# Performance work log

Measured on AMD Instinct MI355X. Metric: run time of the kernel, lower is better.

## Reference

```python
import jax, jax.numpy as jnp
import numpy as np
from jax import lax

B, S, H = 2, 2048, 768
FF = 1536
E = 8
TOP_K = 2


def setup_inputs() -> dict:
    key = jax.random.key(0)
    k1, k2, k3, k4 = jax.random.split(key, 4)
    hidden_states = jax.random.normal(k1, (B, S, H), dtype=jnp.float32)
    # torch init: weight.normal_() for experts; nn.Linear default init for gate (approx normal here is fine for a numerics baseline)
    gate_w = jax.random.normal(k2, (E, H), dtype=jnp.float32) * 0.02
    w_fc = jax.random.normal(k3, (E, FF, H), dtype=jnp.float32) * 0.02
    w_proj = jax.random.normal(k4, (E, H, FF), dtype=jnp.float32) * 0.02
    return {"hidden_states": hidden_states, "gate_w": gate_w, "w_fc": w_fc, "w_proj": w_proj}


def reference(hidden_states, gate_w, w_fc, w_proj):
    b, s, h = hidden_states.shape
    x = hidden_states.reshape(-1, h)                      # [T, H]
    # --- top-k gating (logits in float32, as in the torch code) ---
    logits = (x @ gate_w.T).astype(jnp.float32)           # [T, E]
    top_logits, top_idx = lax.top_k(logits, TOP_K)        # [T, K]
    gates = jax.nn.softmax(top_logits, axis=1).astype(x.dtype)  # [T, K]
    # combined per-token/per-expert gate: g[t,e] = sum_k gates[t,k]*[idx[t,k]==e]
    onehot = jax.nn.one_hot(top_idx, E, dtype=x.dtype)    # [T, K, E]
    g = jnp.einsum('tk,tke->te', gates, onehot)           # [T, E]
    # --- experts: gather + per-expert GEMM + gated scatter-add combine ---
    # Equivalent math: tokens with zero gate for expert e contribute nothing,
    # so compute each expert on all tokens and weight by g[:, e].
    out = jnp.zeros_like(x)
    for e in range(E):  # fixed small loop over experts (structurally distinct weights)
        hmid = jax.nn.gelu(x @ w_fc[e].T, approximate=False)   # [T, FF] (torch gelu = erf form)
        out = out + g[:, e:e + 1] * (hmid @ w_proj[e].T)       # [T, H]
    out = out.reshape(b, s, h)
    return out, logits
```

## Files before the change

### kernel.cpp

```cpp
#include <hip/hip_runtime.h>
#include <hip/hip_bf16.h>
#include <math.h>
#include <stdint.h>

#define TOKENS 4096
#define HDIM   768
#define FFDIM  1536
#define NEXP   8
#define GEMM_GRID 1024
#define SLOTS (GEMM_GRID / 8)

typedef __attribute__((ext_vector_type(8))) short bf16x8;
typedef __attribute__((ext_vector_type(4))) float f32x4;

__device__ __forceinline__ unsigned short f2bf(float f) {
    union { float f; uint32_t u; } c; c.f = f;
    uint32_t u = c.u;
    uint32_t r = (u + 0x7FFFu + ((u >> 16) & 1u)) >> 16;
    return (unsigned short)r;
}

__device__ __forceinline__ void gload_lds16(const void* g, void* l) {
    __builtin_amdgcn_global_load_lds(
        (const __attribute__((address_space(1))) void*)g,
        (__attribute__((address_space(3))) void*)l, 16, 0, 0);
}

__global__ void cast_bf16_2(const float* __restrict__ s1, unsigned short* __restrict__ d1,
                            const float* __restrict__ s2, unsigned short* __restrict__ d2,
                            int n4) {
    int stride = gridDim.x * blockDim.x;
    for (int i = blockIdx.x * blockDim.x + threadIdx.x; i < 2 * n4; i += stride) {
        const float4* s = (i < n4) ? (const float4*)s1 : (const float4*)s2;
        ushort4* d = (i < n4) ? (ushort4*)d1 : (ushort4*)d2;
        int j = (i < n4) ? i : i - n4;
        float4 v = s[j];
        ushort4 o;
        o.x = f2bf(v.x); o.y = f2bf(v.y); o.z = f2bf(v.z); o.w = f2bf(v.w);
        d[j] = o;
    }
}

__global__ __launch_bounds__(256) void gating(
    const float* __restrict__ x, const float* __restrict__ gw,
    float* __restrict__ logits,
    int* __restrict__ tok_e, float* __restrict__ tok_g,
    unsigned short* __restrict__ x_bf, float* __restrict__ outp)
{
    float4 zz = make_float4(0.f, 0.f, 0.f, 0.f);
#pragma unroll
    for (int j = 0; j < 3; j++)
        ((float4*)outp)[blockIdx.x * 768 + j * 256 + threadIdx.x] = zz;

    int t = blockIdx.x * 4 + (threadIdx.x >> 6);
    int lane = threadIdx.x & 63;
    const float4* xt = (const float4*)(x + (size_t)t * HDIM);
    const float4* gw4 = (const float4*)gw;
    ushort4* xbt = (ushort4*)(x_bf + (size_t)t * HDIM);
    float acc[NEXP];
#pragma unroll
    for (int e = 0; e < NEXP; e++) acc[e] = 0.f;
#pragma unroll
    for (int it = 0; it < 3; it++) {
        int i = lane + it * 64;
        float4 xv = xt[i];
        ushort4 o;
        o.x = f2bf(xv.x); o.y = f2bf(xv.y); o.z = f2bf(xv.z); o.w = f2bf(xv.w);
        xbt[i] = o;
#pragma unroll
        for (int e = 0; e < NEXP; e++) {
            float4 wv = gw4[e * 192 + i];
            acc[e] += xv.x * wv.x + xv.y * wv.y + xv.z * wv.z + xv.w * wv.w;
        }
    }
#pragma unroll
    for (int e = 0; e < NEXP; e++) {
#pragma unroll
        for (int off = 32; off > 0; off >>= 1)
            acc[e] += __shfl_xor(acc[e], off);
    }
    if (lane == 0) {
        float4 l0 = make_float4(acc[0], acc[1], acc[2], acc[3]);
        float4 l1 = make_float4(acc[4], acc[5], acc[6], acc[7]);
        float4* lp = (float4*)(logits + (size_t)t * NEXP);
        lp[0] = l0; lp[1] = l1;
        int i0 = 0; float v0 = acc[0];
#pragma unroll
        for (int e = 1; e < NEXP; e++) if (acc[e] > v0) { v0 = acc[e]; i0 = e; }
        int i1 = -1; float v1 = -3.4e38f;
#pragma unroll
        for (int e = 0; e < NEXP; e++) if (e != i0 && acc[e] > v1) { v1 = acc[e]; i1 = e; }
        float g0 = 1.f / (1.f + expf(v1 - v0));
        tok_e[t * 2] = i0; tok_e[t * 2 + 1] = i1;
        tok_g[t * 2] = g0; tok_g[t * 2 + 1] = 1.f - g0;
    }
}

__global__ __launch_bounds__(1024) void build_lists(
    const int* __restrict__ tok_e, const float* __restrict__ tok_g,
    int* __restrict__ counts,
    int* __restrict__ entries, float* __restrict__ gates)
{
    __shared__ unsigned long long wlo[16], whi[16];
    int tid = threadIdx.x;
    int lane = tid & 63, wid = tid >> 6;

    int eL[8]; float gL[8];
    int4 ea = ((const int4*)tok_e)[tid * 2];
    int4 eb = ((const int4*)tok_e)[tid * 2 + 1];
    float4 ga = ((const float4*)tok_g)[tid * 2];
    float4 gb = ((const float4*)tok_g)[tid * 2 + 1];
    eL[0] = ea.x; eL[1] = ea.y; eL[2] = ea.z; eL[3] = ea.w;
    eL[4] = eb.x; eL[5] = eb.y; eL[6] = eb.z; eL[7] = eb.w;
    gL[0] = ga.x; gL[1] = ga.y; gL[2] = ga.z; gL[3] = ga.w;
    gL[4] = gb.x; gL[5] = gb.y; gL[6] = gb.z; gL[7] = gb.w;

    unsigned long long clo = 0, chi = 0;
#pragma unroll
    for (int j = 0; j < 8; j++) {
        int e = eL[j];
        unsigned long long one = 1ull << ((e & 3) * 16);
        if (e < 4) clo += one; else chi += one;
    }
    unsigned long long ilo = clo, ihi = chi;
#pragma unroll
    for (int s = 1; s < 64; s <<= 1) {
        unsigned long long t1 = __shfl_up(ilo, s);
        unsigned long long t2 = __shfl_up(ihi, s);
        if (lane >= s) { ilo += t1; ihi += t2; }
    }
    if (lane == 63) { wlo[wid] = ilo; whi[wid] = ihi; }
    __syncthreads();
    if (tid == 0) {
        unsigned long long rl = 0, rh = 0;
#pragma unroll
        for (int i = 0; i < 16; i++) {
            unsigned long long a = wlo[i], b = whi[i];
            wlo[i] = rl; whi[i] = rh;
            rl += a; rh += b;
        }
#pragma unroll
        for (int e = 0; e < 4; e++) {
            counts[e]     = (int)((rl >> (e * 16)) & 0xFFFF);
            counts[e + 4] = (int)((rh >> (e * 16)) & 0xFFFF);
        }
    }
    __syncthreads();
    unsigned long long rlo = wlo[wid] + (ilo - clo);
    unsigned long long rhi = whi[wid] + (ihi - chi);
#pragma unroll
    for (int j = 0; j < 8; j++) {
        int e = eL[j];
        int sh = (e & 3) * 16;
        unsigned long long one = 1ull << sh;
        int slot;
        if (e < 4) { slot = (int)((rlo >> sh) & 0xFFFF); rlo += one; }
        else       { slot = (int)((rhi >> sh) & 0xFFFF); rhi += one; }
        entries[e * TOKENS + slot] = tid * 8 + j;
        gates[e * TOKENS + slot]   = gL[j];
    }
}

template<int KD, int ND, int TN, int NCTP, bool IS_FC, bool DBUF>
__global__ __launch_bounds__(512) void moe_gemm(
    const unsigned short* __restrict__ Asrc,
    const unsigned short* __restrict__ Bsrc,
    const int* __restrict__ counts,
    const int* __restrict__ entries,
    const float* __restrict__ gates,
    unsigned short* __restrict__ hmid,
    float* __restrict__ outp)
{
    constexpr int BM = 256;
    constexpr int AJ = TN / 32;
    constexpr int CB = TN / 64;
    constexpr int NV = 4 + CB;
    int bkt  = blockIdx.x & 7;
    int slot = blockIdx.x >> 3;

    int cs[NEXP];
#pragma unroll
    for (int e = 0; e < NEXP; e++) cs[e] = counts[e];
    int n_e = cs[bkt];
    int rts = (n_e + BM - 1) >> 8;
    int nfill = rts * NCTP;
    if (slot >= nfill) return;
    int ebase = 0;
#pragma unroll
    for (int e = 0; e < NEXP; e++) if (e < bkt) ebase += cs[e];
    const int* lst = entries + bkt * TOKENS;

    int tid = threadIdx.x;
    int w = tid >> 6;
    int l = tid & 63;
    int sg = l & 7;
    int lr8 = l >> 3;
    int lo = l & 15;
    int q  = l >> 4;
    int wr = w >> 1, wc = w & 1;

    __shared__ __align__(16) unsigned short sA[(DBUF ? 2 : 1) * BM * 64];
    __shared__ __align__(16) unsigned short sB[(DBUF ? 2 : 1) * TN * 64];
    unsigned short* sA0 = sA;
    unsigned short* sA1 = sA + BM * 64;
    unsigned short* sB0 = sB;
    unsigned short* sB1 = sB + TN * 64;

    int aOff[4][2], bOff[AJ][2];
#pragma unroll
    for (int i = 0; i < 4; i++) {
        int m = wr * 64 + i * 16 + lo;
#pragma unroll
        for (int s = 0; s < 2; s++)
            aOff[i][s] = m * 64 + ((s * 4 + q) ^ (m & 7)) * 8;
    }
#pragma unroll
    for (int j = 0; j < AJ; j++) {
        int n = wc * (TN / 2) + j * 16 + lo;
#pragma unroll
        for (int s = 0; s < 2; s++)
            bOff[j][s] = n * 64 + ((s * 4 + q) ^ (n & 7)) * 8;
    }

    for (int p = slot; p < nfill; p += SLOTS) {
        int ct   = p / rts;
        int r    = p - ct * rts;
        int row0 = r << 8;
        int n0 = ct * TN;

        const unsigned short* Ag[4];
        int aLds[4];
#pragma unroll
        for (int c = 0; c < 4; c++) {
            int rr = w * 32 + c * 8 + lr8;
            int gr = row0 + rr;
            int id = gr < n_e ? gr : n_e - 1;
            size_t arow = IS_FC ? (size_t)(lst[id] >> 1) : (size_t)(ebase + id);
            Ag[c] = Asrc + arow * KD + (size_t)((sg ^ (rr & 7)) * 8);
            aLds[c] = (w * 32 + c * 8) * 64;
        }
        const unsigned short* Bg[CB];
        int bLds[CB];
#pragma unroll
        for (int c = 0; c < CB; c++) {
            int rr = w * (TN / 8) + c * 8 + lr8;
            Bg[c] = Bsrc + ((size_t)bkt * ND + n0 + rr) * KD + (size_t)((sg ^ (rr & 7)) * 8);
            bLds[c] = (w * (TN / 8) + c * 8) * 64;
        }

        f32x4 acc[4][AJ];
#pragma unroll
        for (int i = 0; i < 4; i++)
#pragma unroll
            for (int j = 0; j < AJ; j++) acc[i][j] = (f32x4){0.f, 0.f, 0.f, 0.f};

        auto stage = [&](unsigned short* SA, unsigned short* SB, int k0) {
#pragma unroll
            for (int c = 0; c < 4; c++) gload_lds16(Ag[c] + k0, SA + aLds[c]);
#pragma unroll
            for (int c = 0; c < CB; c++) gload_lds16(Bg[c] + k0, SB + bLds[c]);
        };
        auto compute = [&](const unsigned short* SA, const unsigned short* SB) {
#pragma unroll
            for (int s = 0; s < 2; s++) {
                bf16x8 a[4], b[AJ];
#pragma unroll
                for (int i = 0; i < 4; i++) a[i] = *(const bf16x8*)(SA + aOff[i][s]);
#pragma unroll
                for (int j = 0; j < AJ; j++) b[j] = *(const bf16x8*)(SB + bOff[j][s]);
#pragma unroll
                for (int i = 0; i < 4; i++)
#pragma unroll
                    for (int j = 0; j < AJ; j++)
                        acc[i][j] = __builtin_amdgcn_mfma_f32_16x16x32_bf16(a[i], b[j], acc[i][j], 0, 0, 0);
            }
        };

        if constexpr (!DBUF) {
            for (int k0 = 0; k0 < KD; k0 += 64) {
                stage(sA0, sB0, k0);
                __syncthreads();
                compute(sA0, sB0);
                __syncthreads();
            }
        } else {
#define WAITN asm volatile("s_waitcnt vmcnt(%0)" :: "n"(NV) : "memory")
#define WAIT0 asm volatile("s_waitcnt vmcnt(0)" ::: "memory")
            stage(sA0, sB0, 0);
            for (int k0 = 0; k0 < KD; k0 += 128) {
                stage(sA1, sB1, k0 + 64);
                WAITN;
                __builtin_amdgcn_s_barrier();
                __builtin_amdgcn_s_setprio(1);
                compute(sA0, sB0);
                __builtin_amdgcn_s_setprio(0);
                __builtin_amdgcn_s_barrier();
                if (k0 + 128 < KD) {
                    stage(sA0, sB0, k0 + 128);
                    WAITN;
                } else {
                    WAIT0;
                }
                __builtin_amdgcn_s_barrier();
                __builtin_amdgcn_s_setprio(1);
                compute(sA1, sB1);
                __builtin_amdgcn_s_setprio(0);
                __builtin_amdgcn_s_barrier();
            }
#undef WAITN
#undef WAIT0
        }

#pragma unroll
        for (int i = 0; i < 4; i++) {
            int rowB = row0 + wr * 64 + i * 16 + q * 4;
#pragma unroll
            for (int rr = 0; rr < 4; rr++) {
                int orow = rowB + rr;
                if (orow < n_e) {
                    if (IS_FC) {
                        size_t hrow = (size_t)(ebase + orow);
#pragma unroll
                        for (int j = 0; j < AJ; j++) {
                            float v = acc[i][j][rr];
                            v = 0.5f * v * (1.f + erff(v * 0.70710678118654752f));
                            hmid[hrow * ND + n0 + wc * (TN / 2) + j * 16 + lo] = f2bf(v);
                        }
                    } else {
                        int token = lst[orow] >> 1;
                        float g = gates[bkt * TOKENS + orow];
#pragma unroll
                        for (int j = 0; j < AJ; j++) {
                            atomicAdd(&outp[(size_t)token * ND + n0 + wc * (TN / 2) + j * 16 + lo],
                                      acc[i][j][rr] * g);
                        }
                    }
                }
            }
        }
    }
}

extern "C" void kernel_launch(void* const* d_in, const int* in_sizes, int n_in,
                              void* d_out, int out_size, void* d_ws, size_t ws_size,
                              hipStream_t stream) {
    const float* x     = (const float*)d_in[0];
    const float* gw    = (const float*)d_in[1];
    const float* wfc   = (const float*)d_in[2];
    const float* wproj = (const float*)d_in[3];
    float* outp   = (float*)d_out;
    float* logits = outp + (size_t)TOKENS * HDIM;

    char* ws = (char*)d_ws;
    int*   counts  = (int*)ws;
    size_t off = 256;
    int*   entries = (int*)(ws + off);
    float* gates   = (float*)(ws + off + NEXP * TOKENS * 4);
    off += 2ull * NEXP * TOKENS * 4;
    int*   tok_e   = (int*)(ws + off);   off += (size_t)TOKENS * 2 * 4;
    float* tok_g   = (float*)(ws + off); off += (size_t)TOKENS * 2 * 4;
    unsigned short* x_bf   = (unsigned short*)(ws + off); off += (size_t)TOKENS * HDIM * 2;
    unsigned short* wfc_bf = (unsigned short*)(ws + off); off += (size_t)NEXP * FFDIM * HDIM * 2;
    unsigned short* wpj_bf = (unsigned short*)(ws + off); off += (size_t)NEXP * HDIM * FFDIM * 2;
    unsigned short* hmid   = (unsigned short*)(ws + off);

    cast_bf16_2<<<2048, 256, 0, stream>>>(wfc, wfc_bf, wproj, wpj_bf,
                                          NEXP * FFDIM * HDIM / 4);
    gating<<<TOKENS / 4, 256, 0, stream>>>(x, gw, logits, tok_e, tok_g, x_bf, outp);
    build_lists<<<1, 1024, 0, stream>>>(tok_e, tok_g, counts, entries, gates);
    moe_gemm<HDIM, FFDIM, 128, FFDIM / 128, true,  false><<<GEMM_GRID, 512, 0, stream>>>(
        x_bf, wfc_bf, counts, entries, gates, hmid, outp);
    moe_gemm<FFDIM, HDIM, 64,  HDIM / 64,   false, true ><<<GEMM_GRID, 512, 0, stream>>>(
        hmid, wpj_bf, counts, entries, gates, hmid, outp);
}
```

Baseline: 223.0 us.

## Fuse weight cast into gating kernel; double-buffer FC GEMM with BK=32

Merges the weight fp32-to-bf16 cast and the gating kernel into one launch, using extra blocks for the cast, which removes a kernel launch and lets the two run concurrently. It also generalizes the MoE GEMM to a template K-tile size and makes the FC GEMM double-buffered with BK=32 tiles. The smaller tile keeps the doubled LDS footprint in check, and the swizzle is adapted for 4-chunk rows. The cost is more barriers per K step for the FC GEMM, and gating blocks now share the GPU with the bandwidth-heavy cast.

Result: no change. 225.3 us (+1.1%).

```diff
diff --git a/kernel.cpp b/kernel.cpp
--- a/kernel.cpp
+++ b/kernel.cpp
@@ -26,27 +26,27 @@
         (__attribute__((address_space(3))) void*)l, 16, 0, 0);
 }
 
-__global__ void cast_bf16_2(const float* __restrict__ s1, unsigned short* __restrict__ d1,
-                            const float* __restrict__ s2, unsigned short* __restrict__ d2,
-                            int n4) {
-    int stride = gridDim.x * blockDim.x;
-    for (int i = blockIdx.x * blockDim.x + threadIdx.x; i < 2 * n4; i += stride) {
-        const float4* s = (i < n4) ? (const float4*)s1 : (const float4*)s2;
-        ushort4* d = (i < n4) ? (ushort4*)d1 : (ushort4*)d2;
-        int j = (i < n4) ? i : i - n4;
-        float4 v = s[j];
-        ushort4 o;
-        o.x = f2bf(v.x); o.y = f2bf(v.y); o.z = f2bf(v.z); o.w = f2bf(v.w);
-        d[j] = o;
-    }
-}
-
-__global__ __launch_bounds__(256) void gating(
+__global__ __launch_bounds__(256) void cast_gate(
     const float* __restrict__ x, const float* __restrict__ gw,
+    const float* __restrict__ wfc, const float* __restrict__ wproj,
+    unsigned short* __restrict__ wfc_bf, unsigned short* __restrict__ wpj_bf,
     float* __restrict__ logits,
     int* __restrict__ tok_e, float* __restrict__ tok_g,
-    unsigned short* __restrict__ x_bf, float* __restrict__ outp)
+    unsigned short* __restrict__ x_bf, float* __restrict__ outp, int n4)
 {
+    if (blockIdx.x >= 1024) {
+        int stride = 2048 * 256;
+        for (int i = (blockIdx.x - 1024) * 256 + threadIdx.x; i < 2 * n4; i += stride) {
+            const float4* s = (i < n4) ? (const float4*)wfc : (const float4*)wproj;
+            ushort4* d = (i < n4) ? (ushort4*)wfc_bf : (ushort4*)wpj_bf;
+            int j = (i < n4) ? i : i - n4;
+            float4 v = s[j];
+            ushort4 o;
+            o.x = f2bf(v.x); o.y = f2bf(v.y); o.z = f2bf(v.z); o.w = f2bf(v.w);
+            d[j] = o;
+        }
+        return;
+    }
     float4 zz = make_float4(0.f, 0.f, 0.f, 0.f);
 #pragma unroll
     for (int j = 0; j < 3; j++)
@@ -161,7 +161,7 @@
     }
 }
 
-template<int KD, int ND, int TN, int NCTP, bool IS_FC, bool DBUF>
+template<int KD, int ND, int BK, int TN, int NCTP, bool IS_FC>
 __global__ __launch_bounds__(512) void moe_gemm(
     const unsigned short* __restrict__ Asrc,
     const unsigned short* __restrict__ Bsrc,
@@ -173,8 +173,16 @@
 {
     constexpr int BM = 256;
     constexpr int AJ = TN / 32;
-    constexpr int CB = TN / 64;
-    constexpr int NV = 4 + CB;
+    constexpr int S  = BK / 8;
+    constexpr int RPC = 64 / S;
+    constexpr int LS  = (S == 8) ? 3 : 2;
+    constexpr int SH  = (S == 8) ? 0 : 1;
+    constexpr int MK  = S - 1;
+    constexpr int ACAL = 32 / RPC;
+    constexpr int BCAL = (TN / 8) / RPC;
+    constexpr int NV   = ACAL + BCAL;
+    constexpr int SS   = BK / 32;
+
     int bkt  = blockIdx.x & 7;
     int slot = blockIdx.x >> 3;
 
@@ -193,33 +201,33 @@
     int tid = threadIdx.x;
     int w = tid >> 6;
     int l = tid & 63;
-    int sg = l & 7;
-    int lr8 = l >> 3;
+    int sg = l & MK;
+    int lr = l >> LS;
     int lo = l & 15;
     int q  = l >> 4;
     int wr = w >> 1, wc = w & 1;
 
-    __shared__ __align__(16) unsigned short sA[(DBUF ? 2 : 1) * BM * 64];
-    __shared__ __align__(16) unsigned short sB[(DBUF ? 2 : 1) * TN * 64];
+    __shared__ __align__(16) unsigned short sA[2 * BM * BK];
+    __shared__ __align__(16) unsigned short sB[2 * TN * BK];
     unsigned short* sA0 = sA;
-    unsigned short* sA1 = sA + BM * 64;
+    unsigned short* sA1 = sA + BM * BK;
     unsigned short* sB0 = sB;
-    unsigned short* sB1 = sB + TN * 64;
-
-    int aOff[4][2], bOff[AJ][2];
+    unsigned short* sB1 = sB + TN * BK;
+
+    int aOff[4][SS], bOff[AJ][SS];
 #pragma unroll
     for (int i = 0; i < 4; i++) {
         int m = wr * 64 + i * 16 + lo;
 #pragma unroll
-        for (int s = 0; s < 2; s++)
-            aOff[i][s] = m * 64 + ((s * 4 + q) ^ (m & 7)) * 8;
+        for (int s = 0; s < SS; s++)
+            aOff[i][s] = m * BK + (((s * 4 + q) ^ ((m >> SH) & MK)) * 8);
     }
 #pragma unroll
     for (int j = 0; j < AJ; j++) {
         int n = wc * (TN / 2) + j * 16 + lo;
 #pragma unroll
-        for (int s = 0; s < 2; s++)
-            bOff[j][s] = n * 64 + ((s * 4 + q) ^ (n & 7)) * 8;
+        for (int s = 0; s < SS; s++)
+            bOff[j][s] = n * BK + (((s * 4 + q) ^ ((n >> SH) & MK)) * 8);
     }
 
     for (int p = slot; p < nfill; p += SLOTS) {
@@ -228,24 +236,24 @@
         int row0 = r << 8;
         int n0 = ct * TN;
 
-        const unsigned short* Ag[4];
-        int aLds[4];
-#pragma unroll
-        for (int c = 0; c < 4; c++) {
-            int rr = w * 32 + c * 8 + lr8;
+        const unsigned short* Ag[ACAL];
+        int aLds[ACAL];
+#pragma unroll
+        for (int c = 0; c < ACAL; c++) {
+            int rr = w * 32 + c * RPC + lr;
             int gr = row0 + rr;
             int id = gr < n_e ? gr : n_e - 1;
             size_t arow = IS_FC ? (size_t)(lst[id] >> 1) : (size_t)(ebase + id);
-            Ag[c] = Asrc + arow * KD + (size_t)((sg ^ (rr & 7)) * 8);
-            aLds[c] = (w * 32 + c * 8) * 64;
-        }
-        const unsigned short* Bg[CB];
-        int bLds[CB];
-#pragma unroll
-        for (int c = 0; c < CB; c++) {
-            int rr = w * (TN / 8) + c * 8 + lr8;
-            Bg[c] = Bsrc + ((size_t)bkt * ND + n0 + rr) * KD + (size_t)((sg ^ (rr & 7)) * 8);
-            bLds[c] = (w * (TN / 8) + c * 8) * 64;
+            Ag[c] = Asrc + arow * KD + (size_t)((sg ^ ((rr >> SH) & MK)) * 8);
+            aLds[c] = (w * 32 + c * RPC) * BK;
+        }
+        const unsigned short* Bg[BCAL];
+        int bLds[BCAL];
+#pragma unroll
+        for (int c = 0; c < BCAL; c++) {
+            int rr = w * (TN / 8) + c * RPC + lr;
+            Bg[c] = Bsrc + ((size_t)bkt * ND + n0 + rr) * KD + (size_t)((sg ^ ((rr >> SH) & MK)) * 8);
+            bLds[c] = (w * (TN / 8) + c * RPC) * BK;
         }
 
         f32x4 acc[4][AJ];
@@ -256,13 +264,13 @@
 
         auto stage = [&](unsigned short* SA, unsigned short* SB, int k0) {
 #pragma unroll
-            for (int c = 0; c < 4; c++) gload_lds16(Ag[c] + k0, SA + aLds[c]);
-#pragma unroll
-            for (int c = 0; c < CB; c++) gload_lds16(Bg[c] + k0, SB + bLds[c]);
+            for (int c = 0; c < ACAL; c++) gload_lds16(Ag[c] + k0, SA + aLds[c]);
+#pragma unroll
+            for (int c = 0; c < BCAL; c++) gload_lds16(Bg[c] + k0, SB + bLds[c]);
         };
         auto compute = [&](const unsigned short* SA, const unsigned short* SB) {
 #pragma unroll
-            for (int s = 0; s < 2; s++) {
+            for (int s = 0; s < SS; s++) {
                 bf16x8 a[4], b[AJ];
 #pragma unroll
                 for (int i = 0; i < 4; i++) a[i] = *(const bf16x8*)(SA + aOff[i][s]);
@@ -276,40 +284,31 @@
             }
         };
 
-        if constexpr (!DBUF) {
-            for (int k0 = 0; k0 < KD; k0 += 64) {
-                stage(sA0, sB0, k0);
-                __syncthreads();
-                compute(sA0, sB0);
-                __syncthreads();
-            }
-        } else {
 #define WAITN asm volatile("s_waitcnt vmcnt(%0)" :: "n"(NV) : "memory")
 #define WAIT0 asm volatile("s_waitcnt vmcnt(0)" ::: "memory")
-            stage(sA0, sB0, 0);
-            for (int k0 = 0; k0 < KD; k0 += 128) {
-                stage(sA1, sB1, k0 + 64);
+        stage(sA0, sB0, 0);
+        for (int k0 = 0; k0 < KD; k0 += 2 * BK) {
+            stage(sA1, sB1, k0 + BK);
+            WAITN;
+            __builtin_amdgcn_s_barrier();
+            __builtin_amdgcn_s_setprio(1);
+            compute(sA0, sB0);
+            __builtin_amdgcn_s_setprio(0);
+            __builtin_amdgcn_s_barrier();
+            if (k0 + 2 * BK < KD) {
+                stage(sA0, sB0, k0 + 2 * BK);
                 WAITN;
-                __builtin_amdgcn_s_barrier();
-                __builtin_amdgcn_s_setprio(1);
-                compute(sA0, sB0);
-                __builtin_amdgcn_s_setprio(0);
-                __builtin_amdgcn_s_barrier();
-                if (k0 + 128 < KD) {
-                    stage(sA0, sB0, k0 + 128);
-                    WAITN;
-                } else {
-                    WAIT0;
-                }
-                __builtin_amdgcn_s_barrier();
-                __builtin_amdgcn_s_setprio(1);
-                compute(sA1, sB1);
-                __builtin_amdgcn_s_setprio(0);
-                __builtin_amdgcn_s_barrier();
+            } else {
+                WAIT0;
             }
+            __builtin_amdgcn_s_barrier();
+            __builtin_amdgcn_s_setprio(1);
+            compute(sA1, sB1);
+            __builtin_amdgcn_s_setprio(0);
+            __builtin_amdgcn_s_barrier();
+        }
 #undef WAITN
 #undef WAIT0
-        }
 
 #pragma unroll
         for (int i = 0; i < 4; i++) {
@@ -364,12 +363,12 @@
     unsigned short* wpj_bf = (unsigned short*)(ws + off); off += (size_t)NEXP * HDIM * FFDIM * 2;
     unsigned short* hmid   = (unsigned short*)(ws + off);
 
-    cast_bf16_2<<<2048, 256, 0, stream>>>(wfc, wfc_bf, wproj, wpj_bf,
-                                          NEXP * FFDIM * HDIM / 4);
-    gating<<<TOKENS / 4, 256, 0, stream>>>(x, gw, logits, tok_e, tok_g, x_bf, outp);
+    cast_gate<<<3072, 256, 0, stream>>>(x, gw, wfc, wproj, wfc_bf, wpj_bf,
+                                        logits, tok_e, tok_g, x_bf, outp,
+                                        NEXP * FFDIM * HDIM / 4);
     build_lists<<<1, 1024, 0, stream>>>(tok_e, tok_g, counts, entries, gates);
-    moe_gemm<HDIM, FFDIM, 128, FFDIM / 128, true,  false><<<GEMM_GRID, 512, 0, stream>>>(
+    moe_gemm<HDIM, FFDIM, 32, 128, FFDIM / 128, true ><<<GEMM_GRID, 512, 0, stream>>>(
         x_bf, wfc_bf, counts, entries, gates, hmid, outp);
-    moe_gemm<FFDIM, HDIM, 64,  HDIM / 64,   false, true ><<<GEMM_GRID, 512, 0, stream>>>(
+    moe_gemm<FFDIM, HDIM, 64, 64,  HDIM / 64,   false><<<GEMM_GRID, 512, 0, stream>>>(
         hmid, wpj_bf, counts, entries, gates, hmid, outp);
 }
```

## Overlap expert weight casts with list building and FC GEMM via extra blocks

Applied to the files above, without the earlier changes.

The standalone kernel that casts both expert weight tensors to bf16 is removed. The w_fc cast now runs in extra blocks of the list-building kernel, and the w_proj cast runs in extra blocks of the FC GEMM launch, so the bandwidth-bound casts overlap with other work instead of running as a serial pass. The list builder is split into one block per expert, which drops the packed 16-bit counters. The GEMM grids shrink to 768 and 512 working blocks. The cast blocks now compete with GEMM blocks for CUs, and the smaller grids give fewer slots per expert, which could hurt if expert loads are uneven.

Measured after the change: 215.0 us. 1.04x faster.

```diff
diff --git a/kernel.cpp b/kernel.cpp
--- a/kernel.cpp
+++ b/kernel.cpp
@@ -7,8 +7,6 @@
 #define HDIM   768
 #define FFDIM  1536
 #define NEXP   8
-#define GEMM_GRID 1024
-#define SLOTS (GEMM_GRID / 8)
 
 typedef __attribute__((ext_vector_type(8))) short bf16x8;
 typedef __attribute__((ext_vector_type(4))) float f32x4;
@@ -26,19 +24,12 @@
         (__attribute__((address_space(3))) void*)l, 16, 0, 0);
 }
 
-__global__ void cast_bf16_2(const float* __restrict__ s1, unsigned short* __restrict__ d1,
-                            const float* __restrict__ s2, unsigned short* __restrict__ d2,
-                            int n4) {
-    int stride = gridDim.x * blockDim.x;
-    for (int i = blockIdx.x * blockDim.x + threadIdx.x; i < 2 * n4; i += stride) {
-        const float4* s = (i < n4) ? (const float4*)s1 : (const float4*)s2;
-        ushort4* d = (i < n4) ? (ushort4*)d1 : (ushort4*)d2;
-        int j = (i < n4) ? i : i - n4;
-        float4 v = s[j];
-        ushort4 o;
-        o.x = f2bf(v.x); o.y = f2bf(v.y); o.z = f2bf(v.z); o.w = f2bf(v.w);
-        d[j] = o;
-    }
+__device__ __forceinline__ void cast4(const float* __restrict__ s,
+                                      unsigned short* __restrict__ d, int i) {
+    float4 v = ((const float4*)s)[i];
+    ushort4 o;
+    o.x = f2bf(v.x); o.y = f2bf(v.y); o.z = f2bf(v.z); o.w = f2bf(v.w);
+    ((ushort4*)d)[i] = o;
 }
 
 __global__ __launch_bounds__(256) void gating(
@@ -96,12 +87,20 @@
     }
 }
 
-__global__ __launch_bounds__(1024) void build_lists(
+__global__ __launch_bounds__(1024) void build_cast(
     const int* __restrict__ tok_e, const float* __restrict__ tok_g,
     int* __restrict__ counts,
-    int* __restrict__ entries, float* __restrict__ gates)
+    int* __restrict__ entries, float* __restrict__ gates,
+    const float* __restrict__ wfc, unsigned short* __restrict__ wfc_bf, int n4)
 {
-    __shared__ unsigned long long wlo[16], whi[16];
+    if (blockIdx.x >= 8) {
+        int stride = 1024 * 1024;
+        for (int i = (int)(blockIdx.x - 8) * 1024 + threadIdx.x; i < n4; i += stride)
+            cast4(wfc, wfc_bf, i);
+        return;
+    }
+    int e = blockIdx.x;
+    __shared__ unsigned wtot[16], wbase[16];
     int tid = threadIdx.x;
     int lane = tid & 63, wid = tid >> 6;
 
@@ -115,53 +114,38 @@
     gL[0] = ga.x; gL[1] = ga.y; gL[2] = ga.z; gL[3] = ga.w;
     gL[4] = gb.x; gL[5] = gb.y; gL[6] = gb.z; gL[7] = gb.w;
 
-    unsigned long long clo = 0, chi = 0;
-#pragma unroll
-    for (int j = 0; j < 8; j++) {
-        int e = eL[j];
-        unsigned long long one = 1ull << ((e & 3) * 16);
-        if (e < 4) clo += one; else chi += one;
-    }
-    unsigned long long ilo = clo, ihi = chi;
+    unsigned m = 0, cnt = 0;
+#pragma unroll
+    for (int j = 0; j < 8; j++)
+        if (eL[j] == e) { m |= 1u << j; cnt++; }
+
+    unsigned il = cnt;
 #pragma unroll
     for (int s = 1; s < 64; s <<= 1) {
-        unsigned long long t1 = __shfl_up(ilo, s);
-        unsigned long long t2 = __shfl_up(ihi, s);
-        if (lane >= s) { ilo += t1; ihi += t2; }
-    }
-    if (lane == 63) { wlo[wid] = ilo; whi[wid] = ihi; }
+        unsigned t1 = __shfl_up(il, s);
+        if (lane >= s) il += t1;
+    }
+    if (lane == 63) wtot[wid] = il;
     __syncthreads();
     if (tid == 0) {
-        unsigned long long rl = 0, rh = 0;
-#pragma unroll
-        for (int i = 0; i < 16; i++) {
-            unsigned long long a = wlo[i], b = whi[i];
-            wlo[i] = rl; whi[i] = rh;
-            rl += a; rh += b;
-        }
-#pragma unroll
-        for (int e = 0; e < 4; e++) {
-            counts[e]     = (int)((rl >> (e * 16)) & 0xFFFF);
-            counts[e + 4] = (int)((rh >> (e * 16)) & 0xFFFF);
-        }
+        unsigned r = 0;
+#pragma unroll
+        for (int i = 0; i < 16; i++) { unsigned a = wtot[i]; wbase[i] = r; r += a; }
+        counts[e] = (int)r;
     }
     __syncthreads();
-    unsigned long long rlo = wlo[wid] + (ilo - clo);
-    unsigned long long rhi = whi[wid] + (ihi - chi);
+    unsigned slot = wbase[wid] + (il - cnt);
 #pragma unroll
     for (int j = 0; j < 8; j++) {
-        int e = eL[j];
-        int sh = (e & 3) * 16;
-        unsigned long long one = 1ull << sh;
-        int slot;
-        if (e < 4) { slot = (int)((rlo >> sh) & 0xFFFF); rlo += one; }
-        else       { slot = (int)((rhi >> sh) & 0xFFFF); rhi += one; }
-        entries[e * TOKENS + slot] = tid * 8 + j;
-        gates[e * TOKENS + slot]   = gL[j];
-    }
-}
-
-template<int KD, int ND, int TN, int NCTP, bool IS_FC, bool DBUF>
+        if (m & (1u << j)) {
+            entries[e * TOKENS + slot] = tid * 8 + j;
+            gates[e * TOKENS + slot]   = gL[j];
+            slot++;
+        }
+    }
+}
+
+template<int KD, int ND, int TN, int NCTP, int GG, bool IS_FC, bool DBUF>
 __global__ __launch_bounds__(512) void moe_gemm(
     const unsigned short* __restrict__ Asrc,
     const unsigned short* __restrict__ Bsrc,
@@ -169,25 +153,32 @@
     const int* __restrict__ entries,
     const float* __restrict__ gates,
     unsigned short* __restrict__ hmid,
-    float* __restrict__ outp)
+    float* __restrict__ outp,
+    const float* __restrict__ castS, unsigned short* __restrict__ castD, int castN4)
 {
+    if constexpr (IS_FC) {
+        if (blockIdx.x >= GG) {
+            int stride = 512 * 512;
+            for (int i = (int)(blockIdx.x - GG) * 512 + threadIdx.x; i < castN4; i += stride)
+                cast4(castS, castD, i);
+            return;
+        }
+    }
     constexpr int BM = 256;
+    constexpr int SLOTS = GG / 8;
     constexpr int AJ = TN / 32;
     constexpr int CB = TN / 64;
     constexpr int NV = 4 + CB;
     int bkt  = blockIdx.x & 7;
     int slot = blockIdx.x >> 3;
 
-    int cs[NEXP];
-#pragma unroll
-    for (int e = 0; e < NEXP; e++) cs[e] = counts[e];
-    int n_e = cs[bkt];
+    int n_e = counts[bkt];
     int rts = (n_e + BM - 1) >> 8;
     int nfill = rts * NCTP;
     if (slot >= nfill) return;
     int ebase = 0;
 #pragma unroll
-    for (int e = 0; e < NEXP; e++) if (e < bkt) ebase += cs[e];
+    for (int e = 0; e < NEXP; e++) { int c = counts[e]; if (e < bkt) ebase += c; }
     const int* lst = entries + bkt * TOKENS;
 
     int tid = threadIdx.x;
@@ -364,12 +355,15 @@
     unsigned short* wpj_bf = (unsigned short*)(ws + off); off += (size_t)NEXP * HDIM * FFDIM * 2;
     unsigned short* hmid   = (unsigned short*)(ws + off);
 
-    cast_bf16_2<<<2048, 256, 0, stream>>>(wfc, wfc_bf, wproj, wpj_bf,
-                                          NEXP * FFDIM * HDIM / 4);
     gating<<<TOKENS / 4, 256, 0, stream>>>(x, gw, logits, tok_e, tok_g, x_bf, outp);
-    build_lists<<<1, 1024, 0, stream>>>(tok_e, tok_g, counts, entries, gates);
-    moe_gemm<HDIM, FFDIM, 128, FFDIM / 128, true,  false><<<GEMM_GRID, 512, 0, stream>>>(
-        x_bf, wfc_bf, counts, entries, gates, hmid, outp);
-    moe_gemm<FFDIM, HDIM, 64,  HDIM / 64,   false, true ><<<GEMM_GRID, 512, 0, stream>>>(
-        hmid, wpj_bf, counts, entries, gates, hmid, outp);
-}
+    build_cast<<<8 + 1024, 1024, 0, stream>>>(tok_e, tok_g, counts, entries, gates,
+                                              wfc, wfc_bf, NEXP * FFDIM * HDIM / 4);
+    moe_gemm<HDIM, FFDIM, 128, FFDIM / 128, 768, true,  false>
+        <<<768 + 512, 512, 0, stream>>>(
+        x_bf, wfc_bf, counts, entries, gates, hmid, outp,
+        wproj, wpj_bf, NEXP * HDIM * FFDIM / 4);
+    moe_gemm<FFDIM, HDIM, 64,  HDIM / 64,   512, false, true >
+        <<<512, 512, 0, stream>>>(
+        hmid, wpj_bf, counts, entries, gates, hmid, outp,
+        nullptr, nullptr, 0);
+}
```
